# Kernel tuning notes

Measured on AMD Instinct MI355X. Metric: run time of the kernel, lower is better.

## Reference

```python
import jax, jax.numpy as jnp
import numpy as np

EPS = 1e-5
NUM_HEADS = 8
SPLIT = 7


def _ln(x, g, b):
    mu = jnp.mean(x, -1, keepdims=True)
    var = jnp.mean((x - mu) ** 2, -1, keepdims=True)
    return (x - mu) / jnp.sqrt(var + EPS) * g + b


def _lepe_attn(q, k, v, H, W, H_sp, W_sp, num_heads, conv_w, conv_b):
    # q,k,v: [B, H*W, C] (one branch, C = dim//2)
    B, L, C = q.shape
    d = C // num_heads
    scale = d ** -0.5
    nH, nW = H // H_sp, W // W_sp

    def to_win(t):  # [B,L,C] -> [B*nH*nW, heads, H_sp*W_sp, d]
        t = t.reshape(B, nH, H_sp, nW, W_sp, C).transpose(0, 1, 3, 2, 4, 5)
        return t.reshape(-1, H_sp * W_sp, num_heads, d).transpose(0, 2, 1, 3)

    qw, kw = to_win(q), to_win(k)

    # LePE: depthwise 3x3 conv on v inside each window (get_lepe)
    vimg = v.reshape(B, nH, H_sp, nW, W_sp, C).transpose(0, 1, 3, 2, 4, 5)
    vimg = vimg.reshape(-1, H_sp, W_sp, C)  # [nWin, H_sp, W_sp, C]
    lepe = jax.lax.conv_general_dilated(
        vimg, conv_w, (1, 1), 'SAME',
        dimension_numbers=('NHWC', 'HWIO', 'NHWC'),
        feature_group_count=C) + conv_b

    def img2heads(t):  # [nWin,H_sp,W_sp,C] -> [nWin, heads, N, d]
        return t.reshape(-1, H_sp * W_sp, num_heads, d).transpose(0, 2, 1, 3)

    vw = img2heads(vimg)
    lepe = img2heads(lepe)

    attn = jax.nn.softmax(jnp.einsum('whqd,whkd->whqk', qw * scale, kw), axis=-1)
    out = jnp.einsum('whqk,whkd->whqd', attn, vw) + lepe  # [nWin, heads, N, d]

    # windows2img
    out = out.transpose(0, 2, 1, 3).reshape(B, nH, nW, H_sp, W_sp, C)
    out = out.transpose(0, 1, 3, 2, 4, 5).reshape(B, H * W, C)
    return out


def setup_inputs() -> dict:
    key = jax.random.key(0)
    ks = jax.random.split(key, 12)
    B, H, W, C = 8, 56, 56, 256
    hid = 4 * C
    Cb = C // 2  # per-branch channels
    s = 0.02
    return {
        'x': jax.random.normal(ks[0], (B, H * W, C), jnp.float32),
        'H': H,
        'W': W,
        'norm1_g': jnp.ones((C,), jnp.float32),
        'norm1_b': jnp.zeros((C,), jnp.float32),
        'qkv_w': jax.random.normal(ks[1], (C, 3 * C), jnp.float32) * s,
        'proj_w': jax.random.normal(ks[2], (C, C), jnp.float32) * s,
        'proj_b': jnp.zeros((C,), jnp.float32),
        'conv0_w': jax.random.normal(ks[3], (3, 3, 1, Cb), jnp.float32) * s,
        'conv0_b': jnp.zeros((Cb,), jnp.float32),
        'conv1_w': jax.random.normal(ks[4], (3, 3, 1, Cb), jnp.float32) * s,
        'conv1_b': jnp.zeros((Cb,), jnp.float32),
        'norm2_g': jnp.ones((C,), jnp.float32),
        'norm2_b': jnp.zeros((C,), jnp.float32),
        'fc1_w': jax.random.normal(ks[5], (C, hid), jnp.float32) * s,
        'fc1_b': jnp.zeros((hid,), jnp.float32),
        'fc2_w': jax.random.normal(ks[6], (hid, C), jnp.float32) * s,
        'fc2_b': jnp.zeros((C,), jnp.float32),
    }


def reference(x, H, W, norm1_g, norm1_b, qkv_w, proj_w, proj_b,
              conv0_w, conv0_b, conv1_w, conv1_b,
              norm2_g, norm2_b, fc1_w, fc1_b, fc2_w, fc2_b):
    B, L, C = x.shape
    img = _ln(x, norm1_g, norm1_b)
    qkv = (img @ qkv_w).reshape(B, L, 3, C).transpose(2, 0, 1, 3)  # [3,B,L,C]
    h = C // 2
    # branch 0 (idx=0): full-height stripes; branch 1 (idx=1): full-width stripes
    x1 = _lepe_attn(qkv[0, :, :, :h], qkv[1, :, :, :h], qkv[2, :, :, :h],
                    H, W, H, SPLIT, NUM_HEADS // 2, conv0_w, conv0_b)
    x2 = _lepe_attn(qkv[0, :, :, h:], qkv[1, :, :, h:], qkv[2, :, :, h:],
                    H, W, SPLIT, W, NUM_HEADS // 2, conv1_w, conv1_b)
    att = jnp.concatenate([x1, x2], axis=2) @ proj_w + proj_b
    x = x + att
    y = _ln(x, norm2_g, norm2_b)
    y = jax.nn.gelu(y @ fc1_w + fc1_b, approximate=False) @ fc2_w + fc2_b
    return x + y
```

## Files before the change

kernel.cpp:

```cpp
#include <hip/hip_runtime.h>
#include <hip/hip_bf16.h>
#include <math.h>

constexpr int C_DIM = 256;
constexpr int MROWS = 25088;
constexpr int HID   = 1024;

typedef float  f32x4 __attribute__((ext_vector_type(4)));
typedef short  s16x8 __attribute__((ext_vector_type(8)));

__device__ __forceinline__ ushort f2bf(float f) {
    __hip_bfloat16 h = __float2bfloat16(f);
    return *reinterpret_cast<ushort*>(&h);
}
__device__ __forceinline__ unsigned pkbf2(float a, float b) {
    __hip_bfloat162 h = __float22bfloat162_rn(float2{a, b});
    return *reinterpret_cast<unsigned*>(&h);
}
__device__ __forceinline__ float bf2f(ushort u) {
    return __uint_as_float(((unsigned)u) << 16);
}

typedef const __attribute__((address_space(1))) unsigned guint;
typedef __attribute__((address_space(3))) unsigned luint;
__device__ __forceinline__ void gload16(const void* g, void* l) {
    __builtin_amdgcn_global_load_lds((guint*)g, (luint*)l, 16, 0, 0);
}

__global__ __launch_bounds__(256) void ln_kernel(
    const float* __restrict__ x, const float* __restrict__ g,
    const float* __restrict__ b, ushort* __restrict__ out)
{
    int wv = threadIdx.x >> 6, lane = threadIdx.x & 63;
    size_t row = (size_t)blockIdx.x * 4 + wv;
    float4 v = *(const float4*)(x + row * 256 + lane * 4);
    float s1 = v.x + v.y + v.z + v.w;
    float s2 = v.x*v.x + v.y*v.y + v.z*v.z + v.w*v.w;
    #pragma unroll
    for (int d = 1; d < 64; d <<= 1) {
        s1 += __shfl_xor(s1, d);
        s2 += __shfl_xor(s2, d);
    }
    float mu  = s1 * (1.0f / 256.0f);
    float var = s2 * (1.0f / 256.0f) - mu * mu;
    float inv = rsqrtf(var + 1e-5f);
    float4 gv = *(const float4*)(g + lane * 4);
    float4 bv = *(const float4*)(b + lane * 4);
    uint2 o;
    o.x = pkbf2((v.x - mu) * inv * gv.x + bv.x, (v.y - mu) * inv * gv.y + bv.y);
    o.y = pkbf2((v.z - mu) * inv * gv.z + bv.z, (v.w - mu) * inv * gv.w + bv.w);
    *(uint2*)(out + row * 256 + lane * 4) = o;
}

__global__ __launch_bounds__(256) void wcvt_all(
    const float* __restrict__ w0, const float* __restrict__ w1,
    const float* __restrict__ w2, const float* __restrict__ w3,
    ushort* __restrict__ o0, ushort* __restrict__ o1,
    ushort* __restrict__ o2, ushort* __restrict__ o3)
{
    __shared__ ushort tile[64][65];
    int bid = blockIdx.x;
    const float* w; ushort* o; int K, N, tIdx;
    if (bid < 48)       { w = w0; o = o0; K = 256;  N = 768;  tIdx = bid; }
    else if (bid < 64)  { w = w1; o = o1; K = 256;  N = 256;  tIdx = bid - 48; }
    else if (bid < 128) { w = w2; o = o2; K = 256;  N = 1024; tIdx = bid - 64; }
    else                { w = w3; o = o3; K = 1024; N = 256;  tIdx = bid - 128; }
    int nx = N >> 6;
    int bx = tIdx % nx, by = tIdx / nx;
    int n0 = bx * 64, k0 = by * 64;
    int c = threadIdx.x & 63, rr = threadIdx.x >> 6;
    #pragma unroll
    for (int i = 0; i < 64; i += 4) {
        int r = i + rr;
        tile[r][c] = f2bf(w[(size_t)(k0 + r) * N + n0 + c]);
    }
    __syncthreads();
    #pragma unroll
    for (int i = 0; i < 64; i += 4) {
        int r = i + rr;
        o[(size_t)(n0 + r) * K + k0 + c] = tile[c][r];
    }
}

template<int FUSE>
__global__ __launch_bounds__(256) void gemm_bf16(
    const ushort* __restrict__ A, const ushort* __restrict__ Bt,
    const float* __restrict__ bias, const float* res,
    void* Cout, int M, int N, int K)
{
    __shared__ ushort As[128 * 32];
    __shared__ ushort Bs[128 * 32];
    int tid  = threadIdx.x;
    int lane = tid & 63, wv = tid >> 6;
    int lr = lane & 15, lg = lane >> 4;
    int row0 = blockIdx.y * 128, col0 = blockIdx.x * 128;
    int wr = wv >> 1, wc = wv & 1;

    f32x4 acc[4][4];
    #pragma unroll
    for (int m = 0; m < 4; ++m)
        #pragma unroll
        for (int n = 0; n < 4; ++n)
            acc[m][n] = (f32x4){0.f, 0.f, 0.f, 0.f};

    int srow = wv * 32 + (lane >> 2);
    const ushort* gA  = A  + (size_t)(row0 + srow) * K + (lane & 3) * 8;
    const ushort* gA2 = gA + (size_t)16 * K;
    const ushort* gB  = Bt + (size_t)(col0 + srow) * K + (lane & 3) * 8;
    const ushort* gB2 = gB + (size_t)16 * K;
    ushort* lA  = &As[(wv * 32 +  0) * 32];
    ushort* lA2 = &As[(wv * 32 + 16) * 32];
    ushort* lB  = &Bs[(wv * 32 +  0) * 32];
    ushort* lB2 = &Bs[(wv * 32 + 16) * 32];

    for (int k0 = 0; k0 < K; k0 += 32) {
        gload16(gA  + k0, lA);
        gload16(gA2 + k0, lA2);
        gload16(gB  + k0, lB);
        gload16(gB2 + k0, lB2);
        __syncthreads();
        s16x8 af[4], bfg[4];
        #pragma unroll
        for (int m = 0; m < 4; ++m)
            af[m] = *(const s16x8*)&As[(wr * 64 + m * 16 + lr) * 32 + lg * 8];
        #pragma unroll
        for (int n = 0; n < 4; ++n)
            bfg[n] = *(const s16x8*)&Bs[(wc * 64 + n * 16 + lr) * 32 + lg * 8];
        #pragma unroll
        for (int m = 0; m < 4; ++m)
            #pragma unroll
            for (int n = 0; n < 4; ++n)
                acc[m][n] = __builtin_amdgcn_mfma_f32_16x16x32_bf16(af[m], bfg[n], acc[m][n], 0, 0, 0);
        __syncthreads();
    }

    int grow0 = row0 + wr * 64;
    int gcol0 = col0 + wc * 64;
    #pragma unroll
    for (int m = 0; m < 4; ++m) {
        #pragma unroll
        for (int n = 0; n < 4; ++n) {
            int gcol = gcol0 + n * 16 + lr;
            float bv = (FUSE >= 1) ? bias[gcol] : 0.0f;
            #pragma unroll
            for (int r = 0; r < 4; ++r) {
                int grow = grow0 + m * 16 + lg * 4 + r;
                float v = acc[m][n][r] + bv;
                if (FUSE == 2) v = 0.5f * v * (1.0f + erff(v * 0.70710678118654752f));
                if (FUSE == 1) {
                    v += res[(size_t)grow * N + gcol];
                    ((float*)Cout)[(size_t)grow * N + gcol] = v;
                } else {
                    ((ushort*)Cout)[(size_t)grow * N + gcol] = f2bf(v);
                }
            }
        }
    }
}

__device__ __forceinline__ int wrow(int branch, int b, int wi, int n) {
    if (branch) return b * 3136 + wi * 392 + n;
    int ii = n / 7;
    return b * 3136 + ii * 56 + wi * 7 + (n - ii * 7);
}

__global__ __launch_bounds__(512, 2) void attn_kernel(
    const ushort* __restrict__ qkv,
    const float* __restrict__ c0w, const float* __restrict__ c0b,
    const float* __restrict__ c1w, const float* __restrict__ c1b,
    ushort* __restrict__ att)
{
    __shared__ ushort Kh[2 * 416 * 16];
    __shared__ ushort Vt[32][424];
    __shared__ ushort Pl[8][16][40];
    __shared__ float  CwS[9][32];
    __shared__ float  CbS[32];

    int bid    = blockIdx.x;
    int branch = bid >> 8;
    int rem    = bid & 255;
    int head   = rem & 3;
    int win    = rem >> 2;
    int b  = win >> 3, wi = win & 7;
    int c0 = branch * 128 + head * 32;
    const float* cw = branch ? c1w : c0w;
    const float* cb = branch ? c1b : c0b;
    int tid = threadIdx.x;

    if (tid < 288) {
        int tap = tid >> 5, d = tid & 31;
        CwS[tap][d] = cw[tap * 128 + head * 32 + d];
    } else if (tid < 320) {
        CbS[tid - 288] = cb[head * 32 + (tid - 288)];
    }
    for (int e = tid; e < 1664; e += 512) {
        int n = e >> 2, quad = e & 3;
        uint4 v = make_uint4(0u, 0u, 0u, 0u);
        if (n < 392) {
            int gr = wrow(branch, b, wi, n);
            v = *(const uint4*)(qkv + (size_t)gr * 768 + 256 + c0 + quad * 8);
        }
        *(uint4*)&Kh[(quad >> 1) * 6656 + n * 16 + (quad & 1) * 8] = v;
    }
    for (int e = tid; e < 1568; e += 512) {
        int n = e >> 2, quad = e & 3;
        int gr = wrow(branch, b, wi, n);
        uint4 v = *(const uint4*)(qkv + (size_t)gr * 768 + 512 + c0 + quad * 8);
        const ushort* us = (const ushort*)&v;
        #pragma unroll
        for (int j = 0; j < 8; ++j) Vt[quad * 8 + j][n] = us[j];
    }
    for (int e = tid; e < 1024; e += 512) {
        int d = e >> 5, k = 392 + (e & 31);
        Vt[d][k] = 0;
    }
    __syncthreads();

    int wv = tid >> 6, lane = tid & 63;
    int lr = lane & 15, lg = lane >> 4;
    constexpr float kSc = 0.17677669529663689f * 1.4426950408889634f;
    ushort* Pw = &Pl[wv][0][0];
    int Hsp = branch ? 7 : 56, Wsp = branch ? 56 : 7;
    const ushort* Kbase = &Kh[(lg >> 1) * 6656 + lr * 16 + (lg & 1) * 8];

    for (int qt = wv; qt < 25; qt += 8) {
        int q0 = qt * 16;
        int qn = q0 + lr; if (qn > 391) qn = 391;
        int qr = wrow(branch, b, wi, qn);
        s16x8 qf = *(const s16x8*)(qkv + (size_t)qr * 768 + c0 + lg * 8);

        f32x4 o0 = {0.f, 0.f, 0.f, 0.f}, o1 = {0.f, 0.f, 0.f, 0.f};
        float psum = 0.0f;

        auto do_chunk = [&](int c, bool last) {
            f32x4 z = {0.f, 0.f, 0.f, 0.f};
            s16x8 kf0 = *(const s16x8*)&Kbase[(c * 32)      * 16];
            s16x8 kf1 = *(const s16x8*)&Kbase[(c * 32 + 16) * 16];
            f32x4 s0 = __builtin_amdgcn_mfma_f32_16x16x32_bf16(kf0, qf, z, 0, 0, 0);
            f32x4 s1 = __builtin_amdgcn_mfma_f32_16x16x32_bf16(kf1, qf, z, 0, 0, 0);
            float p[2][4];
            #pragma unroll
            for (int r = 0; r < 4; ++r) {
                p[0][r] = exp2f(s0[r] * kSc);
                p[1][r] = exp2f(s1[r] * kSc);
            }
            if (last) {
                #pragma unroll
                for (int t = 0; t < 2; ++t)
                    #pragma unroll
                    for (int r = 0; r < 4; ++r) {
                        int kk = 384 + t * 16 + lg * 4 + r;
                        if (kk >= 392) p[t][r] = 0.0f;
                    }
            }
            #pragma unroll
            for (int t = 0; t < 2; ++t)
                #pragma unroll
                for (int r = 0; r < 4; ++r) psum += p[t][r];
            uint2 w0, w1;
            w0.x = pkbf2(p[0][0], p[0][1]); w0.y = pkbf2(p[0][2], p[0][3]);
            w1.x = pkbf2(p[1][0], p[1][1]); w1.y = pkbf2(p[1][2], p[1][3]);
            *(uint2*)&Pw[lr * 40 + lg * 4]      = w0;
            *(uint2*)&Pw[lr * 40 + 16 + lg * 4] = w1;
            s16x8 pf = *(const s16x8*)&Pw[lr * 40 + lg * 8];
            s16x8 v0 = *(const s16x8*)&Vt[lr][c * 32 + lg * 8];
            s16x8 v1 = *(const s16x8*)&Vt[16 + lr][c * 32 + lg * 8];
            o0 = __builtin_amdgcn_mfma_f32_16x16x32_bf16(pf, v0, o0, 0, 0, 0);
            o1 = __builtin_amdgcn_mfma_f32_16x16x32_bf16(pf, v1, o1, 0, 0, 0);
        };

        for (int c = 0; c < 12; ++c) do_chunk(c, false);
        do_chunk(12, true);

        psum += __shfl_xor(psum, 16);
        psum += __shfl_xor(psum, 32);
        float linv[4];
        #pragma unroll
        for (int r = 0; r < 4; ++r)
            linv[r] = 1.0f / __shfl(psum, lg * 4 + r);
        #pragma unroll
        for (int r = 0; r < 4; ++r) { o0[r] *= linv[r]; o1[r] *= linv[r]; }

        #pragma unroll
        for (int r = 0; r < 4; ++r) {
            int q = q0 + lg * 4 + r;
            if (q >= 392) continue;
            int ii = branch ? (q / 56) : (q / 7);
            int jj = q - ii * Wsp;
            float a0 = o0[r], a1 = o1[r];
            #pragma unroll
            for (int kh = 0; kh < 3; ++kh) {
                int i2 = ii + kh - 1;
                if ((unsigned)i2 >= (unsigned)Hsp) continue;
                #pragma unroll
                for (int kw = 0; kw < 3; ++kw) {
                    int j2 = jj + kw - 1;
                    if ((unsigned)j2 >= (unsigned)Wsp) continue;
                    int pos = i2 * Wsp + j2;
                    a0 += CwS[kh * 3 + kw][lr]      * bf2f(Vt[lr][pos]);
                    a1 += CwS[kh * 3 + kw][16 + lr] * bf2f(Vt[16 + lr][pos]);
                }
            }
            a0 += CbS[lr]; a1 += CbS[16 + lr];
            int gr = wrow(branch, b, wi, q);
            att[(size_t)gr * 256 + branch * 128 + head * 32 + lr]      = f2bf(a0);
            att[(size_t)gr * 256 + branch * 128 + head * 32 + 16 + lr] = f2bf(a1);
        }
    }
}

extern "C" void kernel_launch(void* const* d_in, const int* in_sizes, int n_in,
                              void* d_out, int out_size, void* d_ws, size_t ws_size,
                              hipStream_t stream)
{
    const float* x      = (const float*)d_in[0];
    const float* n1g    = (const float*)d_in[3];
    const float* n1b    = (const float*)d_in[4];
    const float* qkv_w  = (const float*)d_in[5];
    const float* proj_w = (const float*)d_in[6];
    const float* proj_b = (const float*)d_in[7];
    const float* c0w    = (const float*)d_in[8];
    const float* c0b    = (const float*)d_in[9];
    const float* c1w    = (const float*)d_in[10];
    const float* c1b    = (const float*)d_in[11];
    const float* n2g    = (const float*)d_in[12];
    const float* n2b    = (const float*)d_in[13];
    const float* fc1_w  = (const float*)d_in[14];
    const float* fc1_b  = (const float*)d_in[15];
    const float* fc2_w  = (const float*)d_in[16];
    const float* fc2_b  = (const float*)d_in[17];
    float* out = (float*)d_out;

    char* ws = (char*)d_ws;
    const size_t SZ_BF = (size_t)MROWS * C_DIM * 2;
    ushort* img  = (ushort*)(ws);
    ushort* att  = (ushort*)(ws + SZ_BF);
    ushort* big  = (ushort*)(ws + 2 * SZ_BF);
    char*   wbase = ws + 2 * SZ_BF + (size_t)MROWS * HID * 2;
    ushort* qkvT = (ushort*)(wbase);
    ushort* projT= (ushort*)(wbase +  393216);
    ushort* fc1T = (ushort*)(wbase +  393216 + 131072);
    ushort* fc2T = (ushort*)(wbase +  393216 + 131072 + 524288);

    wcvt_all<<<192, 256, 0, stream>>>(qkv_w, proj_w, fc1_w, fc2_w, qkvT, projT, fc1T, fc2T);

    ln_kernel<<<MROWS / 4, 256, 0, stream>>>(x, n1g, n1b, img);
    gemm_bf16<0><<<dim3(768 / 128, MROWS / 128), 256, 0, stream>>>(
        img, qkvT, nullptr, nullptr, big, MROWS, 768, 256);
    attn_kernel<<<512, 512, 0, stream>>>(big, c0w, c0b, c1w, c1b, att);
    gemm_bf16<1><<<dim3(256 / 128, MROWS / 128), 256, 0, stream>>>(
        att, projT, proj_b, x, out, MROWS, 256, 256);
    ln_kernel<<<MROWS / 4, 256, 0, stream>>>(out, n2g, n2b, img);
    gemm_bf16<2><<<dim3(HID / 128, MROWS / 128), 256, 0, stream>>>(
        img, fc1T, fc1_b, nullptr, big, MROWS, HID, 256);
    gemm_bf16<1><<<dim3(256 / 128, MROWS / 128), 256, 0, stream>>>(
        big, fc2T, fc2_b, out, out, MROWS, 256, 1024);
}
```

Measured before the change: 334.4 us.

## Double-buffer GEMM LDS tiles, remap blocks per XCD, vectorize epilogue, fast GELU

The GEMM kernel now double-buffers its LDS tiles so the next K-slice's global-to-LDS load is issued before the current slice's MFMAs run. Block IDs are remapped so consecutive tiles land on the same XCD, which is meant to improve L2 reuse. The MFMA operands are swapped so each lane holds 4 consecutive columns, which allows float4/uint2 vectorized epilogue stores and bias loads. Exact erf GELU is replaced by a tanh approximation, which changes numerics slightly.

```diff
diff --git a/kernel.cpp b/kernel.cpp
--- a/kernel.cpp
+++ b/kernel.cpp
@@ -19,6 +19,13 @@
 }
 __device__ __forceinline__ float bf2f(ushort u) {
     return __uint_as_float(((unsigned)u) << 16);
+}
+
+__device__ __forceinline__ float fast_gelu(float v) {
+    float u = v * (0.7978845608028654f + 0.035677408136f * v * v);
+    float e = __expf(2.0f * u);
+    float t = 1.0f - 2.0f / (e + 1.0f);
+    return 0.5f * v * (1.0f + t);
 }
 
 typedef const __attribute__((address_space(1))) unsigned guint;
@@ -86,73 +93,98 @@
 __global__ __launch_bounds__(256) void gemm_bf16(
     const ushort* __restrict__ A, const ushort* __restrict__ Bt,
     const float* __restrict__ bias, const float* res,
-    void* Cout, int M, int N, int K)
-{
-    __shared__ ushort As[128 * 32];
-    __shared__ ushort Bs[128 * 32];
+    void* Cout, int M, int N, int K, int NBX)
+{
+    __shared__ ushort As[2][128 * 32];
+    __shared__ ushort Bs[2][128 * 32];
     int tid  = threadIdx.x;
     int lane = tid & 63, wv = tid >> 6;
     int lr = lane & 15, lg = lane >> 4;
-    int row0 = blockIdx.y * 128, col0 = blockIdx.x * 128;
+
+    int nwg = gridDim.x;
+    int qc = nwg >> 3, rc = nwg & 7;
+    int xcd = blockIdx.x & 7, pos = blockIdx.x >> 3;
+    int wg = (xcd < rc ? xcd * (qc + 1) : rc * (qc + 1) + (xcd - rc) * qc) + pos;
+    int row0 = (wg / NBX) * 128, col0 = (wg % NBX) * 128;
     int wr = wv >> 1, wc = wv & 1;
 
     f32x4 acc[4][4];
     #pragma unroll
-    for (int m = 0; m < 4; ++m)
-        #pragma unroll
-        for (int n = 0; n < 4; ++n)
-            acc[m][n] = (f32x4){0.f, 0.f, 0.f, 0.f};
+    for (int n = 0; n < 4; ++n)
+        #pragma unroll
+        for (int m = 0; m < 4; ++m)
+            acc[n][m] = (f32x4){0.f, 0.f, 0.f, 0.f};
 
     int srow = wv * 32 + (lane >> 2);
     const ushort* gA  = A  + (size_t)(row0 + srow) * K + (lane & 3) * 8;
     const ushort* gA2 = gA + (size_t)16 * K;
     const ushort* gB  = Bt + (size_t)(col0 + srow) * K + (lane & 3) * 8;
     const ushort* gB2 = gB + (size_t)16 * K;
-    ushort* lA  = &As[(wv * 32 +  0) * 32];
-    ushort* lA2 = &As[(wv * 32 + 16) * 32];
-    ushort* lB  = &Bs[(wv * 32 +  0) * 32];
-    ushort* lB2 = &Bs[(wv * 32 + 16) * 32];
-
-    for (int k0 = 0; k0 < K; k0 += 32) {
-        gload16(gA  + k0, lA);
-        gload16(gA2 + k0, lA2);
-        gload16(gB  + k0, lB);
-        gload16(gB2 + k0, lB2);
+
+#define STAGE(buf, k0) do {                                      \
+        gload16(gA  + (k0), &As[buf][(wv * 32 +  0) * 32]);      \
+        gload16(gA2 + (k0), &As[buf][(wv * 32 + 16) * 32]);      \
+        gload16(gB  + (k0), &Bs[buf][(wv * 32 +  0) * 32]);      \
+        gload16(gB2 + (k0), &Bs[buf][(wv * 32 + 16) * 32]);      \
+    } while (0)
+
+#define COMPUTE(buf) do {                                                          \
+        s16x8 af[4], bfg[4];                                                       \
+        _Pragma("unroll")                                                          \
+        for (int m = 0; m < 4; ++m)                                                \
+            af[m] = *(const s16x8*)&As[buf][(wr * 64 + m * 16 + lr) * 32 + lg * 8];\
+        _Pragma("unroll")                                                          \
+        for (int n = 0; n < 4; ++n)                                                \
+            bfg[n] = *(const s16x8*)&Bs[buf][(wc * 64 + n * 16 + lr) * 32 + lg * 8];\
+        _Pragma("unroll")                                                          \
+        for (int n = 0; n < 4; ++n)                                                \
+            _Pragma("unroll")                                                      \
+            for (int m = 0; m < 4; ++m)                                            \
+                acc[n][m] = __builtin_amdgcn_mfma_f32_16x16x32_bf16(               \
+                    bfg[n], af[m], acc[n][m], 0, 0, 0);                            \
+    } while (0)
+
+    STAGE(0, 0);
+    __syncthreads();
+    #pragma unroll 1
+    for (int k0 = 0; k0 + 64 <= K; k0 += 64) {
+        STAGE(1, k0 + 32);
+        COMPUTE(0);
         __syncthreads();
-        s16x8 af[4], bfg[4];
-        #pragma unroll
-        for (int m = 0; m < 4; ++m)
-            af[m] = *(const s16x8*)&As[(wr * 64 + m * 16 + lr) * 32 + lg * 8];
-        #pragma unroll
-        for (int n = 0; n < 4; ++n)
-            bfg[n] = *(const s16x8*)&Bs[(wc * 64 + n * 16 + lr) * 32 + lg * 8];
-        #pragma unroll
-        for (int m = 0; m < 4; ++m)
-            #pragma unroll
-            for (int n = 0; n < 4; ++n)
-                acc[m][n] = __builtin_amdgcn_mfma_f32_16x16x32_bf16(af[m], bfg[n], acc[m][n], 0, 0, 0);
+        if (k0 + 64 < K) STAGE(0, k0 + 64);
+        COMPUTE(1);
         __syncthreads();
     }
+#undef STAGE
+#undef COMPUTE
 
     int grow0 = row0 + wr * 64;
     int gcol0 = col0 + wc * 64;
     #pragma unroll
-    for (int m = 0; m < 4; ++m) {
-        #pragma unroll
-        for (int n = 0; n < 4; ++n) {
-            int gcol = gcol0 + n * 16 + lr;
-            float bv = (FUSE >= 1) ? bias[gcol] : 0.0f;
-            #pragma unroll
-            for (int r = 0; r < 4; ++r) {
-                int grow = grow0 + m * 16 + lg * 4 + r;
-                float v = acc[m][n][r] + bv;
-                if (FUSE == 2) v = 0.5f * v * (1.0f + erff(v * 0.70710678118654752f));
-                if (FUSE == 1) {
-                    v += res[(size_t)grow * N + gcol];
-                    ((float*)Cout)[(size_t)grow * N + gcol] = v;
-                } else {
-                    ((ushort*)Cout)[(size_t)grow * N + gcol] = f2bf(v);
-                }
+    for (int n = 0; n < 4; ++n) {
+        int gcol = gcol0 + n * 16 + lg * 4;
+        float4 b4 = make_float4(0.f, 0.f, 0.f, 0.f);
+        if (FUSE >= 1) b4 = *(const float4*)&bias[gcol];
+        #pragma unroll
+        for (int m = 0; m < 4; ++m) {
+            int grow = grow0 + m * 16 + lr;
+            float v0 = acc[n][m][0] + b4.x;
+            float v1 = acc[n][m][1] + b4.y;
+            float v2 = acc[n][m][2] + b4.z;
+            float v3 = acc[n][m][3] + b4.w;
+            if (FUSE == 2) {
+                v0 = fast_gelu(v0); v1 = fast_gelu(v1);
+                v2 = fast_gelu(v2); v3 = fast_gelu(v3);
+            }
+            if (FUSE == 1) {
+                const float4 rr = *(const float4*)&res[(size_t)grow * N + gcol];
+                float4 o = make_float4(v0 + rr.x, v1 + rr.y, v2 + rr.z, v3 + rr.w);
+                *(float4*)&((float*)Cout)[(size_t)grow * N + gcol] = o;
+            } else {
+                uint2 o;
+                o.x = pkbf2(v0, v1);
+                o.y = pkbf2(v2, v3);
+                *(uint2*)&((ushort*)Cout)[(size_t)grow * N + gcol] = o;
             }
         }
     }
@@ -345,14 +377,14 @@
     wcvt_all<<<192, 256, 0, stream>>>(qkv_w, proj_w, fc1_w, fc2_w, qkvT, projT, fc1T, fc2T);
 
     ln_kernel<<<MROWS / 4, 256, 0, stream>>>(x, n1g, n1b, img);
-    gemm_bf16<0><<<dim3(768 / 128, MROWS / 128), 256, 0, stream>>>(
-        img, qkvT, nullptr, nullptr, big, MROWS, 768, 256);
+    gemm_bf16<0><<<196 * 6, 256, 0, stream>>>(
+        img, qkvT, nullptr, nullptr, big, MROWS, 768, 256, 6);
     attn_kernel<<<512, 512, 0, stream>>>(big, c0w, c0b, c1w, c1b, att);
-    gemm_bf16<1><<<dim3(256 / 128, MROWS / 128), 256, 0, stream>>>(
-        att, projT, proj_b, x, out, MROWS, 256, 256);
+    gemm_bf16<1><<<196 * 2, 256, 0, stream>>>(
+        att, projT, proj_b, x, out, MROWS, 256, 256, 2);
     ln_kernel<<<MROWS / 4, 256, 0, stream>>>(out, n2g, n2b, img);
-    gemm_bf16<2><<<dim3(HID / 128, MROWS / 128), 256, 0, stream>>>(
-        img, fc1T, fc1_b, nullptr, big, MROWS, HID, 256);
-    gemm_bf16<1><<<dim3(256 / 128, MROWS / 128), 256, 0, stream>>>(
-        big, fc2T, fc2_b, out, out, MROWS, 256, 1024);
-}
+    gemm_bf16<2><<<196 * 8, 256, 0, stream>>>(
+        img, fc1T, fc1_b, nullptr, big, MROWS, HID, 256, 8);
+    gemm_bf16<1><<<196 * 2, 256, 0, stream>>>(
+        big, fc2T, fc2_b, out, out, MROWS, 256, 1024, 2);
+}
```

Result: faster. 312.6 us (-6.5%).
